# Kernel optimization log

Hardware: AMD Instinct MI355X
Metric: run time of the kernel (lower is better)

The kernel has to match this reference:

```python
import jax, jax.numpy as jnp
import numpy as np

B, L, H, S, IN = 64, 64, 128, 64, 16  # batch, embedding_seq_len, hidden, seq_num, input_size


def setup_inputs() -> dict:
    key = jax.random.key(0)
    k = jax.random.split(key, 8)
    trip = jax.random.normal(k[0], (B, 256, IN), dtype=jnp.float32)
    valid_len = jax.random.randint(k[1], (B,), 0, 256)
    embedding = jax.random.normal(k[2], (B, L, H), dtype=jnp.float32)
    # gates: Linear(2H -> 4H), xavier-uniform weight
    lim_g = float(np.sqrt(6.0 / (2 * H + 4 * H)))
    W_gates = jax.random.uniform(k[3], (2 * H, 4 * H), minval=-lim_g, maxval=lim_g, dtype=jnp.float32)
    b_gates = jax.random.uniform(k[4], (4 * H,), minval=-1.0 / np.sqrt(2 * H), maxval=1.0 / np.sqrt(2 * H), dtype=jnp.float32)
    # linear: Linear(H -> input_size)
    lim_l = float(np.sqrt(6.0 / (H + IN)))
    W_lin = jax.random.uniform(k[5], (H, IN), minval=-lim_l, maxval=lim_l, dtype=jnp.float32)
    b_lin = jax.random.uniform(k[6], (IN,), minval=-1.0 / np.sqrt(H), maxval=1.0 / np.sqrt(H), dtype=jnp.float32)
    return {"trip": trip, "valid_len": valid_len, "embedding": embedding,
            "W_gates": W_gates, "b_gates": b_gates, "W_lin": W_lin, "b_lin": b_lin}


def _gate_update(inp, c, W_gates, b_gates):
    g = inp @ W_gates + b_gates
    f, i, o, cand = jnp.split(g, 4, axis=-1)
    c_new = jax.nn.sigmoid(f) * c + jax.nn.sigmoid(i) * jnp.tanh(cand)  # broadcasts [B,1,H] vs [B,L,H] at step 0
    h_new = jax.nn.sigmoid(o) * jnp.tanh(c_new)
    return c_new, h_new


def reference(trip, valid_len, embedding, W_gates, b_gates, W_lin, b_lin):
    x = trip  # sampler pass-through
    b, l, h = embedding.shape
    c0 = jnp.zeros((b, l, h), dtype=embedding.dtype)
    h0 = jnp.zeros((b, l, h), dtype=embedding.dtype)
    # step 0: gates on [embedding[:, :1], h[:, :1]] -> [B,1,4H], broadcast update
    inp0 = jnp.concatenate([embedding[:, :1, :], h0[:, :1, :]], axis=-1)
    c1, h1 = _gate_update(inp0, c0, W_gates, b_gates)

    def step(carry, _):
        c, hh = carry
        inp = jnp.concatenate([c, hh], axis=-1)  # [B,L,2H]
        c_new, h_new = _gate_update(inp, c, W_gates, b_gates)
        return (c_new, h_new), c_new

    (_, _), cs = jax.lax.scan(step, (c1, h1), None, length=S - 1)  # cs: [S-1,B,L,H]
    c_all = jnp.concatenate([c1[None], cs], axis=0)          # [S,B,L,H]
    c_all = jnp.transpose(c_all, (1, 0, 2, 3)).reshape(b, S * l, h)  # cat along dim=-2
    out = c_all @ W_lin + b_lin  # [B, S*L, IN]
    return (x, out)
```

## Files before the change

### kernel.cpp

```cpp
#include <hip/hip_runtime.h>

typedef _Float16 f16x8 __attribute__((ext_vector_type(8)));
typedef float f32x4 __attribute__((ext_vector_type(4)));

#define HDIM  128
#define NSTEP 64
#define NG    512
#define BPB   16

#define LOG2E 1.44269504088896340736f

__device__ __forceinline__ float rcpf(float x) { return __builtin_amdgcn_rcpf(x); }
__device__ __forceinline__ float exp2neg(float x) {
    float r; asm("v_exp_f32 %0, -%1" : "=v"(r) : "v"(x)); return r;
}
__device__ __forceinline__ unsigned int packh2(float a, float b) {
    union { _Float16 h[2]; unsigned int u; } x;
    x.h[0] = (_Float16)a; x.h[1] = (_Float16)b; return x.u;
}

__global__ __launch_bounds__(256) void copy_trip_k(const float4* __restrict__ src,
                                                   float4* __restrict__ dst) {
    int i = blockIdx.x * 256 + threadIdx.x;
    dst[i] = src[i];
}

__global__ __launch_bounds__(512, 2) void recur_k(
    const float* __restrict__ emb, const float* __restrict__ Wg,
    const float* __restrict__ bg,  float* __restrict__ outb) {
    __shared__ __align__(16) unsigned int state_s[2][BPB * 128];

    const int blk = blockIdx.x, t = threadIdx.x;
    const int w = t >> 6, l = t & 63;
    const int lg = l >> 4, lr = l & 15;
    const int h = w * 16 + lr;

    f16x8 B[4][8];
    f32x4 bias4[4];
    #pragma unroll
    for (int i = 0; i < 4; ++i) {
        const float sc = (i == 3) ? 2.f * LOG2E : LOG2E;
        const int c = i * 128 + h;
        const float bb = bg[c] * sc;
        bias4[i] = (f32x4){bb, bb, bb, bb};
        #pragma unroll
        for (int kt = 0; kt < 8; ++kt) {
            f16x8 v;
            #pragma unroll
            for (int e = 0; e < 8; ++e) {
                const int k = kt * 32 + lg * 8 + e;
                const int r = (k & 1) ? 128 + (k >> 1) : (k >> 1);
                v[e] = (_Float16)(Wg[r * NG + c] * sc);
            }
            B[i][kt] = v;
        }
    }
    #pragma unroll
    for (int i = 0; i < 4; ++i)
        #pragma unroll
        for (int kt = 0; kt < 8; ++kt)
            asm volatile("" : "+a"(B[i][kt]));

    for (int wd = t; wd < BPB * 128; wd += 512) {
        int batch = wd >> 7, kw = wd & 127;
        float ev = emb[(size_t)(blk * BPB + batch) * 64 * HDIM + kw];
        *(unsigned int*)((char*)state_s[0] + batch * 512 + ((kw * 4) ^ ((batch & 7) << 4)))
            = packh2(ev, 0.f);
    }
    float c[4] = {0.f, 0.f, 0.f, 0.f};
    float ph[4];
    int hoff[4];
    #pragma unroll
    for (int q = 0; q < 4; ++q)
        hoff[q] = (blk * BPB + lg * 4 + q) * 65536 + h;
    __syncthreads();

    #pragma unroll 2
    for (int s = 0; s < NSTEP; ++s) {
        const char* buf = (const char*)state_s[s & 1];
        f16x8 a8[8];
        #pragma unroll
        for (int kt = 0; kt < 8; ++kt)
            a8[kt] = *(const f16x8*)(buf + lr * 512 + ((kt * 64 + lg * 16) ^ ((lr & 7) << 4)));
        if (s > 0) {
            float* ob = outb + (size_t)(s - 1) * 1024;
            #pragma unroll
            for (int q = 0; q < 4; ++q) ob[hoff[q]] = ph[q];
        }
        f32x4 acc[4];
        #pragma unroll
        for (int i = 0; i < 4; ++i)
            asm("v_mfma_f32_16x16x32_f16 %0, %1, %2, %3"
                : "=v"(acc[i]) : "v"(a8[0]), "a"(B[i][0]), "v"(bias4[i]));
        #pragma unroll
        for (int kt = 1; kt < 8; ++kt) {
            #pragma unroll
            for (int i = 0; i < 4; ++i)
                asm("v_mfma_f32_16x16x32_f16 %0, %1, %2, %0"
                    : "+v"(acc[i]) : "v"(a8[kt]), "a"(B[i][kt]));
        }
        char* bufn = (char*)state_s[(s + 1) & 1];
        #pragma unroll
        for (int q = 0; q < 4; ++q) {
            float F = rcpf(1.f + exp2neg(acc[0][q]));
            float I = rcpf(1.f + exp2neg(acc[1][q]));
            float O = rcpf(1.f + exp2neg(acc[2][q]));
            float Dd = fmaf(2.f, rcpf(1.f + exp2neg(acc[3][q])), -1.f);
            float cn = fmaf(F, c[q], I * Dd);
            float th = fmaf(2.f, rcpf(1.f + exp2neg(cn * (2.f * LOG2E))), -1.f);
            float hn = O * th;
            c[q] = cn; ph[q] = cn;
            const int batch = lg * 4 + q;
            *(unsigned int*)(bufn + batch * 512 + ((4 * h) ^ ((batch & 7) << 4)))
                = packh2(cn, hn);
        }
        __syncthreads();
    }
    {
        float* ob = outb + (size_t)63 * 1024;
        #pragma unroll
        for (int q = 0; q < 4; ++q) ob[hoff[q]] = ph[q];
    }
}

__global__ __launch_bounds__(256) void proj_expand_k(const float* __restrict__ Wl,
                                                     const float* __restrict__ bl,
                                                     float* __restrict__ outb) {
    __shared__ float c_s[HDIM];
    __shared__ __align__(16) float pj[16];
    const int bs = blockIdx.x, t = threadIdx.x;
    float* reg = outb + (size_t)bs * 1024;
    if (t < HDIM) c_s[t] = reg[t];
    __syncthreads();
    if (t < 16) {
        float a = bl[t];
        #pragma unroll 16
        for (int h = 0; h < HDIM; ++h) a = fmaf(c_s[h], Wl[h * 16 + t], a);
        pj[t] = a;
    }
    __syncthreads();
    float4 v = ((const float4*)pj)[t & 3];
    ((float4*)reg)[t] = v;
}

extern "C" void kernel_launch(void* const* d_in, const int* in_sizes, int n_in,
                              void* d_out, int out_size, void* d_ws, size_t ws_size,
                              hipStream_t stream) {
    const float* trip = (const float*)d_in[0];
    const float* emb  = (const float*)d_in[2];
    const float* Wg   = (const float*)d_in[3];
    const float* bgp  = (const float*)d_in[4];
    const float* Wlp  = (const float*)d_in[5];
    const float* blp  = (const float*)d_in[6];
    float* out = (float*)d_out;

    copy_trip_k<<<256, 256, 0, stream>>>((const float4*)trip, (float4*)out);
    recur_k<<<4, 512, 0, stream>>>(emb, Wg, bgp, out + 262144);
    proj_expand_k<<<4096, 256, 0, stream>>>(Wlp, blp, out + 262144);
}
```

Measured before the change: 90.21 us.

## Split recurrence over 8 blocks of 8 batches and fold trip copy into projection

Result: faster. 76.31 us (-15.4%).

```diff
diff --git a/kernel.cpp b/kernel.cpp
--- a/kernel.cpp
+++ b/kernel.cpp
@@ -6,7 +6,8 @@
 #define HDIM  128
 #define NSTEP 64
 #define NG    512
-#define BPB   16
+#define NBLK  8
+#define BPB   8
 
 #define LOG2E 1.44269504088896340736f
 
@@ -19,12 +20,6 @@
     x.h[0] = (_Float16)a; x.h[1] = (_Float16)b; return x.u;
 }
 
-__global__ __launch_bounds__(256) void copy_trip_k(const float4* __restrict__ src,
-                                                   float4* __restrict__ dst) {
-    int i = blockIdx.x * 256 + threadIdx.x;
-    dst[i] = src[i];
-}
-
 __global__ __launch_bounds__(512, 2) void recur_k(
     const float* __restrict__ emb, const float* __restrict__ Wg,
     const float* __restrict__ bg,  float* __restrict__ outb) {
@@ -34,6 +29,7 @@
     const int w = t >> 6, l = t & 63;
     const int lg = l >> 4, lr = l & 15;
     const int h = w * 16 + lr;
+    const int mr = lr & 7;
 
     f16x8 B[4][8];
     f32x4 bias4[4];
@@ -67,12 +63,15 @@
         *(unsigned int*)((char*)state_s[0] + batch * 512 + ((kw * 4) ^ ((batch & 7) << 4)))
             = packh2(ev, 0.f);
     }
-    float c[4] = {0.f, 0.f, 0.f, 0.f};
-    float ph[4];
-    int hoff[4];
+
+    const int b_base = (lg & 1) * 4 + (lg >> 1) * 2;
+    const bool hi = (lg >= 2);
+    float c2[2] = {0.f, 0.f};
+    float ph2[2];
+    int hoff[2];
     #pragma unroll
-    for (int q = 0; q < 4; ++q)
-        hoff[q] = (blk * BPB + lg * 4 + q) * 65536 + h;
+    for (int j = 0; j < 2; ++j)
+        hoff[j] = (blk * BPB + b_base + j) * 65536 + h;
     __syncthreads();
 
     #pragma unroll 2
@@ -81,36 +80,38 @@
         f16x8 a8[8];
         #pragma unroll
         for (int kt = 0; kt < 8; ++kt)
-            a8[kt] = *(const f16x8*)(buf + lr * 512 + ((kt * 64 + lg * 16) ^ ((lr & 7) << 4)));
+            a8[kt] = *(const f16x8*)(buf + mr * 512 + ((kt * 64 + lg * 16) ^ ((mr & 7) << 4)));
         if (s > 0) {
             float* ob = outb + (size_t)(s - 1) * 1024;
             #pragma unroll
-            for (int q = 0; q < 4; ++q) ob[hoff[q]] = ph[q];
+            for (int j = 0; j < 2; ++j) ob[hoff[j]] = ph2[j];
         }
         f32x4 acc[4];
         #pragma unroll
-        for (int i = 0; i < 4; ++i)
-            asm("v_mfma_f32_16x16x32_f16 %0, %1, %2, %3"
-                : "=v"(acc[i]) : "v"(a8[0]), "a"(B[i][0]), "v"(bias4[i]));
+        for (int i = 0; i < 4; ++i) acc[i] = bias4[i];
+        asm volatile("s_nop 3");
         #pragma unroll
-        for (int kt = 1; kt < 8; ++kt) {
+        for (int kt = 0; kt < 8; ++kt) {
             #pragma unroll
             for (int i = 0; i < 4; ++i)
-                asm("v_mfma_f32_16x16x32_f16 %0, %1, %2, %0"
+                asm volatile("v_mfma_f32_16x16x32_f16 %0, %1, %2, %0"
                     : "+v"(acc[i]) : "v"(a8[kt]), "a"(B[i][kt]));
         }
+        asm volatile("s_nop 7\n\ts_nop 7");
+        __builtin_amdgcn_sched_barrier(0);
         char* bufn = (char*)state_s[(s + 1) & 1];
         #pragma unroll
-        for (int q = 0; q < 4; ++q) {
-            float F = rcpf(1.f + exp2neg(acc[0][q]));
-            float I = rcpf(1.f + exp2neg(acc[1][q]));
-            float O = rcpf(1.f + exp2neg(acc[2][q]));
-            float Dd = fmaf(2.f, rcpf(1.f + exp2neg(acc[3][q])), -1.f);
-            float cn = fmaf(F, c[q], I * Dd);
+        for (int j = 0; j < 2; ++j) {
+            const int qa = hi ? 2 + j : j;
+            float F = rcpf(1.f + exp2neg(acc[0][qa]));
+            float I = rcpf(1.f + exp2neg(acc[1][qa]));
+            float O = rcpf(1.f + exp2neg(acc[2][qa]));
+            float Dd = fmaf(2.f, rcpf(1.f + exp2neg(acc[3][qa])), -1.f);
+            float cn = fmaf(F, c2[j], I * Dd);
             float th = fmaf(2.f, rcpf(1.f + exp2neg(cn * (2.f * LOG2E))), -1.f);
             float hn = O * th;
-            c[q] = cn; ph[q] = cn;
-            const int batch = lg * 4 + q;
+            c2[j] = cn; ph2[j] = cn;
+            const int batch = b_base + j;
             *(unsigned int*)(bufn + batch * 512 + ((4 * h) ^ ((batch & 7) << 4)))
                 = packh2(cn, hn);
         }
@@ -119,16 +120,23 @@
     {
         float* ob = outb + (size_t)63 * 1024;
         #pragma unroll
-        for (int q = 0; q < 4; ++q) ob[hoff[q]] = ph[q];
+        for (int j = 0; j < 2; ++j) ob[hoff[j]] = ph2[j];
     }
 }
 
 __global__ __launch_bounds__(256) void proj_expand_k(const float* __restrict__ Wl,
                                                      const float* __restrict__ bl,
+                                                     const float* __restrict__ trip,
+                                                     float* __restrict__ trip_out,
                                                      float* __restrict__ outb) {
+    const int bs = blockIdx.x, t = threadIdx.x;
+    if (bs >= 4096) {
+        int i = (bs - 4096) * 256 + t;
+        ((float4*)trip_out)[i] = ((const float4*)trip)[i];
+        return;
+    }
     __shared__ float c_s[HDIM];
     __shared__ __align__(16) float pj[16];
-    const int bs = blockIdx.x, t = threadIdx.x;
     float* reg = outb + (size_t)bs * 1024;
     if (t < HDIM) c_s[t] = reg[t];
     __syncthreads();
@@ -154,7 +162,6 @@
     const float* blp  = (const float*)d_in[6];
     float* out = (float*)d_out;
 
-    copy_trip_k<<<256, 256, 0, stream>>>((const float4*)trip, (float4*)out);
-    recur_k<<<4, 512, 0, stream>>>(emb, Wg, bgp, out + 262144);
-    proj_expand_k<<<4096, 256, 0, stream>>>(Wlp, blp, out + 262144);
+    recur_k<<<NBLK, 512, 0, stream>>>(emb, Wg, bgp, out + 262144);
+    proj_expand_k<<<4096 + 256, 256, 0, stream>>>(Wlp, blp, trip, out, out + 262144);
 }
```
